# Kernel tuning notes

Hardware: AMD Instinct MI355X
Metric: run time of the kernel (lower is better)

## Reference

```python
import jax, jax.numpy as jnp
import numpy as np

WINDOW = 512
OVERLAP = 64
STRIDE = WINDOW - OVERLAP  # 448
HEADS = 12
HEAD_DIM = 3072 // HEADS  # 256
SCALE = 1.0 / np.sqrt(HEAD_DIM)


def setup_inputs() -> dict:
    key = jax.random.key(0)
    ks = jax.random.split(key, 9)
    B, S, H = 1, 8192, 3072
    w = 0.02  # weight init scale
    return {
        "hidden_states": jax.random.normal(ks[0], (B, S, H), jnp.float32),
        "Wq": jax.random.normal(ks[1], (H, H), jnp.float32) * w,
        "bq": jnp.zeros((H,), jnp.float32),
        "Wk": jax.random.normal(ks[2], (H, H), jnp.float32) * w,
        "bk": jnp.zeros((H,), jnp.float32),
        "Wv": jax.random.normal(ks[3], (H, H), jnp.float32) * w,
        "bv": jnp.zeros((H,), jnp.float32),
        "Wo": jax.random.normal(ks[4], (H, H), jnp.float32) * w,
        "bo": jnp.zeros((H,), jnp.float32),
    }


def reference(hidden_states, Wq, bq, Wk, bk, Wv, bv, Wo, bo):
    B, S, H = hidden_states.shape
    n_win = -(-S // STRIDE)  # ceil: windows start at 0, STRIDE, 2*STRIDE, ... < S
    starts = np.arange(n_win) * STRIDE                      # static
    idx = starts[:, None] + np.arange(WINDOW)[None, :]      # [n_win, W]
    valid = jnp.asarray(idx < S)                            # [n_win, W] bool
    idx_c = np.minimum(idx, S - 1)                          # clamp for gather

    # Gather overlapping windows: [B, n_win, W, H] (redundant QKV on overlap, as in original)
    win = hidden_states[:, idx_c]

    def proj(Wm, bm):
        y = jnp.einsum('bnwh,oh->bnwo', win, Wm) + bm
        return y.reshape(B, n_win, WINDOW, HEADS, HEAD_DIM)

    q = proj(Wq, bq)
    k = proj(Wk, bk)
    v = proj(Wv, bv)

    scores = jnp.einsum('bnqhd,bnkhd->bnhqk', q, k) * SCALE  # [B,n_win,heads,W,W]
    # Padded (out-of-range) key positions of the short last window must not attend
    scores = jnp.where(valid[None, :, None, None, :], scores, -1e9)
    attn = jax.nn.softmax(scores, axis=-1)
    ctx = jnp.einsum('bnhqk,bnkhd->bnqhd', attn, v)
    ctx = ctx.reshape(B, n_win, WINDOW, H)
    out_w = jnp.einsum('bnwh,oh->bnwo', ctx, Wo) + bo        # [B,n_win,W,H]

    # zero padded query rows, then overlap-add + average
    out_w = out_w * valid[None, :, :, None].astype(out_w.dtype)
    flat_idx = jnp.asarray(idx_c.reshape(-1))                # [n_win*W]
    output = jnp.zeros((B, S, H), out_w.dtype).at[:, flat_idx].add(
        out_w.reshape(B, -1, H))
    counts = jnp.zeros((S,), out_w.dtype).at[flat_idx].add(
        valid.reshape(-1).astype(out_w.dtype))
    return output / jnp.maximum(counts, 1.0)[None, :, None]
```

## Files before the change

kernel.cpp:

```cpp
#include <hip/hip_runtime.h>
#include <hip/hip_bf16.h>
#include <stdint.h>

#define SEQ   8192
#define HDIM  3072
#define NWIN  19
#define WINL  512
#define STR   448
#define NHEAD 12
#define DHEAD 256
#define QKVN  9216
#define ATTN_SCALE 0.0625f

typedef unsigned short u16;
typedef __bf16 bf16x8 __attribute__((ext_vector_type(8)));
typedef float  f32x4  __attribute__((ext_vector_type(4)));
typedef unsigned short us8 __attribute__((ext_vector_type(8)));

__device__ __forceinline__ u16 f2b(float x) {
  return __builtin_bit_cast(u16, __float2bfloat16(x));
}
__device__ __forceinline__ float b2f(u16 u) {
  return __builtin_bit_cast(float, (unsigned int)(u) << 16);
}
__device__ __forceinline__ void gload_lds16(const void* g, void* l) {
  __builtin_amdgcn_global_load_lds(
      (const __attribute__((address_space(1))) void*)g,
      (__attribute__((address_space(3))) void*)l, 16, 0, 0);
}

__global__ __launch_bounds__(256) void cvt_f32_bf16(const float* __restrict__ src,
                                                    u16* __restrict__ dst, int n8) {
  int i = blockIdx.x * 256 + threadIdx.x;
  if (i >= n8) return;
  const float4* s4 = (const float4*)src;
  float4 a = s4[2 * i], b = s4[2 * i + 1];
  us8 o;
  o[0] = f2b(a.x); o[1] = f2b(a.y); o[2] = f2b(a.z); o[3] = f2b(a.w);
  o[4] = f2b(b.x); o[5] = f2b(b.y); o[6] = f2b(b.z); o[7] = f2b(b.w);
  *((us8*)dst + i) = o;
}

__global__ __launch_bounds__(256) void biascat(const float* __restrict__ bq,
                                               const float* __restrict__ bk,
                                               const float* __restrict__ bv,
                                               float* __restrict__ dst) {
  int i = blockIdx.x * 256 + threadIdx.x;
  if (i >= QKVN) return;
  dst[i] = (i < HDIM) ? bq[i] : ((i < 2 * HDIM) ? bk[i - HDIM] : bv[i - 2 * HDIM]);
}

template <bool BF16OUT>
__global__ __launch_bounds__(512, 2) void gemm256(const u16* __restrict__ A,
                                                  const u16* __restrict__ B,
                                                  const float* __restrict__ bias,
                                                  float* __restrict__ outF,
                                                  u16* __restrict__ outB,
                                                  int N, int K) {
  __shared__ __align__(16) u16 As[2][2][128][64];
  __shared__ __align__(16) u16 Bs[2][2][128][64];
  const int tid = threadIdx.x;
  const int w = tid >> 6, l = tid & 63;
  const int wm = w >> 2, wn = w & 3;
  const int fr = l & 15, g = l >> 4;
  const int xcd = blockIdx.x & 7, loc = blockIdx.x >> 3;
  const int bn = loc >> 2, bm = xcd * 4 + (loc & 3);

  const int srow = tid >> 3;
  const int lc = (tid & 7) ^ ((tid >> 3) & 7);
  const u16* sA0 = A + (size_t)(bm * 256 + srow) * K + lc * 8;
  const u16* sA1 = sA0 + (size_t)64 * K;
  const u16* sB0 = B + (size_t)(bn * 256 + srow) * K + lc * 8;
  const u16* sB1 = sB0 + (size_t)64 * K;
  const size_t hiK = (size_t)128 * K;
  const int t16 = tid * 16;
  char* Aw = (char*)As;
  char* Bw = (char*)Bs;

  int rbA[4], rbB[2], ck[2];
#pragma unroll
  for (int i = 0; i < 4; ++i) rbA[i] = (i * 32 + wm * 16 + fr) * 128;
  rbB[0] = (wn * 16 + fr) * 128;
  rbB[1] = (64 + wn * 16 + fr) * 128;
  ck[0] = ((g) ^ (fr & 7)) * 16;
  ck[1] = ((4 + g) ^ (fr & 7)) * 16;

  f32x4 acc[8][4];
#pragma unroll
  for (int i = 0; i < 8; ++i)
#pragma unroll
    for (int j = 0; j < 4; ++j) acc[i][j] = (f32x4){0.f, 0.f, 0.f, 0.f};

  gload_lds16(sA0, Aw + t16); gload_lds16(sA1, Aw + 8192 + t16);
  gload_lds16(sB0, Bw + t16); gload_lds16(sB1, Bw + 8192 + t16);
  gload_lds16(sB0 + hiK, Bw + 16384 + t16); gload_lds16(sB1 + hiK, Bw + 16384 + 8192 + t16);
  gload_lds16(sA0 + hiK, Aw + 16384 + t16); gload_lds16(sA1 + hiK, Aw + 16384 + 8192 + t16);
  sA0 += 64; sA1 += 64; sB0 += 64; sB1 += 64;
  asm volatile("s_waitcnt vmcnt(4)" ::: "memory");
  __builtin_amdgcn_s_barrier();
  __builtin_amdgcn_sched_barrier(0);

  const int NT = K >> 6;
  for (int T = 0; T < NT; ++T) {
    const int cur = T & 1, pp = (T + 1) & 1;
    const bool ds = (T + 1 < NT);
    const bool last = (T == NT - 1);
    const char* ah = (const char*)As + cur * 32768;
    const char* bh = (const char*)Bs + cur * 32768;
    char* apw = Aw + pp * 32768;
    char* bpw = Bw + pp * 32768;
    bf16x8 af[4][2], bf[4][2];

#pragma unroll
    for (int mi = 0; mi < 4; ++mi)
#pragma unroll
      for (int kk = 0; kk < 2; ++kk)
        af[mi][kk] = *(const bf16x8*)(ah + rbA[mi] + ck[kk]);
#pragma unroll
    for (int ni = 0; ni < 2; ++ni)
#pragma unroll
      for (int kk = 0; kk < 2; ++kk)
        bf[ni][kk] = *(const bf16x8*)(bh + rbB[ni] + ck[kk]);
    if (ds) { gload_lds16(sA0, apw + t16); gload_lds16(sA1, apw + 8192 + t16); }
    __builtin_amdgcn_s_barrier();
    asm volatile("s_waitcnt lgkmcnt(0)" ::: "memory");
    __builtin_amdgcn_s_setprio(1);
#pragma unroll
    for (int kk = 0; kk < 2; ++kk)
#pragma unroll
      for (int mi = 0; mi < 4; ++mi)
#pragma unroll
        for (int ni = 0; ni < 2; ++ni)
          acc[mi][ni] = __builtin_amdgcn_mfma_f32_16x16x32_bf16(af[mi][kk], bf[ni][kk], acc[mi][ni], 0, 0, 0);
    __builtin_amdgcn_s_setprio(0);
    if (last) asm volatile("s_waitcnt vmcnt(2)" ::: "memory");
    else      asm volatile("s_waitcnt vmcnt(4)" ::: "memory");
    __builtin_amdgcn_s_barrier();

#pragma unroll
    for (int ni = 2; ni < 4; ++ni)
#pragma unroll
      for (int kk = 0; kk < 2; ++kk)
        bf[ni][kk] = *(const bf16x8*)(bh + 16384 + rbB[ni - 2] + ck[kk]);
    if (ds) { gload_lds16(sB0, bpw + t16); gload_lds16(sB1, bpw + 8192 + t16); }
    __builtin_amdgcn_s_barrier();
    asm volatile("s_waitcnt lgkmcnt(0)" ::: "memory");
    __builtin_amdgcn_s_setprio(1);
#pragma unroll
    for (int kk = 0; kk < 2; ++kk)
#pragma unroll
      for (int mi = 0; mi < 4; ++mi)
#pragma unroll
        for (int ni = 2; ni < 4; ++ni)
          acc[mi][ni] = __builtin_amdgcn_mfma_f32_16x16x32_bf16(af[mi][kk], bf[ni][kk], acc[mi][ni], 0, 0, 0);
    __builtin_amdgcn_s_setprio(0);
    if (last) asm volatile("s_waitcnt vmcnt(0)" ::: "memory");
    else      asm volatile("s_waitcnt vmcnt(4)" ::: "memory");
    __builtin_amdgcn_s_barrier();

#pragma unroll
    for (int mi = 0; mi < 4; ++mi)
#pragma unroll
      for (int kk = 0; kk < 2; ++kk)
        af[mi][kk] = *(const bf16x8*)(ah + 16384 + rbA[mi] + ck[kk]);
    if (ds) { gload_lds16(sB0 + hiK, bpw + 16384 + t16); gload_lds16(sB1 + hiK, bpw + 16384 + 8192 + t16); }
    __builtin_amdgcn_s_barrier();
    asm volatile("s_waitcnt lgkmcnt(0)" ::: "memory");
    __builtin_amdgcn_s_setprio(1);
#pragma unroll
    for (int kk = 0; kk < 2; ++kk)
#pragma unroll
      for (int mi = 0; mi < 4; ++mi)
#pragma unroll
        for (int ni = 0; ni < 2; ++ni)
          acc[mi + 4][ni] = __builtin_amdgcn_mfma_f32_16x16x32_bf16(af[mi][kk], bf[ni][kk], acc[mi + 4][ni], 0, 0, 0);
    __builtin_amdgcn_s_setprio(0);
    __builtin_amdgcn_s_barrier();

    if (ds) { gload_lds16(sA0 + hiK, apw + 16384 + t16); gload_lds16(sA1 + hiK, apw + 16384 + 8192 + t16); }
    __builtin_amdgcn_s_barrier();
    __builtin_amdgcn_s_setprio(1);
#pragma unroll
    for (int kk = 0; kk < 2; ++kk)
#pragma unroll
      for (int mi = 0; mi < 4; ++mi)
#pragma unroll
        for (int ni = 2; ni < 4; ++ni)
          acc[mi + 4][ni] = __builtin_amdgcn_mfma_f32_16x16x32_bf16(af[mi][kk], bf[ni][kk], acc[mi + 4][ni], 0, 0, 0);
    __builtin_amdgcn_s_setprio(0);
    if (!last) asm volatile("s_waitcnt vmcnt(4)" ::: "memory");
    __builtin_amdgcn_s_barrier();
    if (ds) { sA0 += 64; sA1 += 64; sB0 += 64; sB1 += 64; }
    __builtin_amdgcn_sched_barrier(0);
  }

#pragma unroll
  for (int ni = 0; ni < 4; ++ni) {
    const int c = bn * 256 + ni * 64 + wn * 16 + fr;
    const float bvv = bias ? bias[c] : 0.0f;
#pragma unroll
    for (int mi = 0; mi < 8; ++mi) {
      const int r0 = bm * 256 + mi * 32 + wm * 16 + g * 4;
#pragma unroll
      for (int jj = 0; jj < 4; ++jj) {
        float v = acc[mi][ni][jj] + bvv;
        if (BF16OUT) outB[(size_t)(r0 + jj) * N + c] = f2b(v);
        else         outF[(size_t)(r0 + jj) * N + c] = v;
      }
    }
  }
}

__global__ __launch_bounds__(256) void vtrans(const u16* __restrict__ QKV,
                                              u16* __restrict__ Vt) {
  __shared__ u16 t[64][72];
  const int tid = threadIdx.x;
  const int s0 = blockIdx.x * 64, c0 = blockIdx.y * 64;
  {
    const int r2 = tid >> 3, cc = (tid & 7) * 8;
#pragma unroll
    for (int p = 0; p < 2; ++p) {
      const int row = r2 + p * 32;
      u16 tmp[8];
      *(uint4*)tmp = *(const uint4*)(QKV + (size_t)(s0 + row) * QKVN + 2 * HDIM + c0 + cc);
#pragma unroll
      for (int j = 0; j < 8; ++j) t[row][cc + j] = tmp[j];
    }
  }
  __syncthreads();
  {
    const int cr2 = tid >> 3, sc = tid & 7;
#pragma unroll
    for (int p = 0; p < 2; ++p) {
      const int c = cr2 + p * 32;
      u16 tmp[8];
#pragma unroll
      for (int j = 0; j < 8; ++j) tmp[j] = t[sc * 8 + j][c];
      *(uint4*)(Vt + (size_t)(c0 + c) * SEQ + s0 + sc * 8) = *(uint4*)tmp;
    }
  }
}

__global__ __launch_bounds__(256, 2) void attn_kernel(const u16* __restrict__ QKV,
                                                      const u16* __restrict__ Vt,
                                                      u16* __restrict__ ctxw) {
  __shared__ __align__(16) u16 Ks[64 * 256];
  __shared__ __align__(16) u16 Vts[256 * 64];
  __shared__ __align__(16) u16 Ps[4][16 * 64];
  const int qb = blockIdx.x, h = blockIdx.y, n = blockIdx.z;
  const int tid = threadIdx.x, w = tid >> 6, l = tid & 63;
  const int g = l >> 4, fr = l & 15;
  const int s0 = n * STR;

  bf16x8 qf[8];
  {
    int sq = s0 + qb * 64 + w * 16 + fr;
    if (sq > SEQ - 1) sq = SEQ - 1;
    const u16* qbase = QKV + (size_t)sq * QKVN + h * DHEAD + g * 8;
#pragma unroll
    for (int dc = 0; dc < 8; ++dc) qf[dc] = *(const bf16x8*)(qbase + dc * 32);
  }
  f32x4 ctx[16];
#pragma unroll
  for (int dn = 0; dn < 16; ++dn) ctx[dn] = (f32x4){0.f, 0.f, 0.f, 0.f};
  float mrow[4] = {-3e38f, -3e38f, -3e38f, -3e38f};
  float lrow[4] = {0.f, 0.f, 0.f, 0.f};

  const int kr_in = l >> 5;
  const int kcp = l & 31;
  const int vr_in = l >> 3;
  const int vcp = l & 7;

  for (int kt = 0; kt < 8; ++kt) {
    const int sb = s0 + kt * 64;
#pragma unroll
    for (int i = 0; i < 8; ++i) {
      const int c = i * 4 + w;
      {
        const int krow = c * 2 + kr_in;
        const int cl = kcp ^ (krow & 31);
        int sk = sb + krow;
        if (sk > SEQ - 1) sk = SEQ - 1;
        gload_lds16(QKV + (size_t)sk * QKVN + HDIM + h * DHEAD + cl * 8, (char*)Ks + c * 1024);
      }
      {
        const int d = c * 8 + vr_in;
        const int cl = vcp ^ (d & 7);
        int sv = sb + cl * 8;
        if (sv > SEQ - 8) sv = SEQ - 8;
        gload_lds16(Vt + (size_t)(h * DHEAD + d) * SEQ + sv, (char*)Vts + c * 1024);
      }
    }
    __syncthreads();

    f32x4 sacc[4];
#pragma unroll
    for (int kn = 0; kn < 4; ++kn) sacc[kn] = (f32x4){0.f, 0.f, 0.f, 0.f};
#pragma unroll
    for (int kn = 0; kn < 4; ++kn) {
      const int krow = kn * 16 + fr;
      const char* krp = (const char*)Ks + krow * 512;
      const int rx = krow & 31;
#pragma unroll
      for (int dc = 0; dc < 8; ++dc) {
        bf16x8 kf = *(const bf16x8*)(krp + (((dc * 4 + g) ^ rx) << 4));
        sacc[kn] = __builtin_amdgcn_mfma_f32_16x16x32_bf16(qf[dc], kf, sacc[kn], 0, 0, 0);
      }
    }
    float mt[4];
#pragma unroll
    for (int kn = 0; kn < 4; ++kn) {
      const bool valid = (sb + kn * 16 + fr) < SEQ;
#pragma unroll
      for (int r = 0; r < 4; ++r) {
        float v = valid ? sacc[kn][r] * ATTN_SCALE : -1e9f;
        sacc[kn][r] = v;
        mt[r] = (kn == 0) ? v : fmaxf(mt[r], v);
      }
    }
#pragma unroll
    for (int r = 0; r < 4; ++r) {
#pragma unroll
      for (int off = 1; off < 16; off <<= 1)
        mt[r] = fmaxf(mt[r], __shfl_xor(mt[r], off, 64));
    }
    float corr[4];
#pragma unroll
    for (int r = 0; r < 4; ++r) {
      float mnew = fmaxf(mrow[r], mt[r]);
      corr[r] = __expf(mrow[r] - mnew);
      mrow[r] = mnew;
    }
    float psum[4] = {0.f, 0.f, 0.f, 0.f};
    char* pw = (char*)&Ps[w][0];
#pragma unroll
    for (int kn = 0; kn < 4; ++kn) {
#pragma unroll
      for (int r = 0; r < 4; ++r) {
        float p = __expf(sacc[kn][r] - mrow[r]);
        psum[r] += p;
        const int q = g * 4 + r;
        *(u16*)(pw + q * 128 + ((2 * (kn * 16 + fr)) ^ ((q & 7) << 4))) = f2b(p);
      }
    }
#pragma unroll
    for (int r = 0; r < 4; ++r) {
#pragma unroll
      for (int off = 1; off < 16; off <<= 1)
        psum[r] += __shfl_xor(psum[r], off, 64);
      lrow[r] = lrow[r] * corr[r] + psum[r];
    }
#pragma unroll
    for (int dn = 0; dn < 16; ++dn)
#pragma unroll
      for (int r = 0; r < 4; ++r) ctx[dn][r] *= corr[r];
    __syncthreads();

    bf16x8 pf[2];
#pragma unroll
    for (int kc = 0; kc < 2; ++kc)
      pf[kc] = *(const bf16x8*)(pw + fr * 128 + ((kc * 64 + g * 16) ^ ((fr & 7) << 4)));
#pragma unroll
    for (int dn = 0; dn < 16; ++dn) {
      const int d = dn * 16 + fr;
      const char* vrp = (const char*)Vts + d * 128;
      const int dx = d & 7;
#pragma unroll
      for (int kc = 0; kc < 2; ++kc) {
        bf16x8 vf = *(const bf16x8*)(vrp + (((kc * 4 + g) ^ dx) << 4));
        ctx[dn] = __builtin_amdgcn_mfma_f32_16x16x32_bf16(pf[kc], vf, ctx[dn], 0, 0, 0);
      }
    }
    __syncthreads();
  }
  float inv[4];
#pragma unroll
  for (int r = 0; r < 4; ++r) inv[r] = 1.0f / lrow[r];
  const int qrow0 = qb * 64 + w * 16 + g * 4;
#pragma unroll
  for (int dn = 0; dn < 16; ++dn) {
#pragma unroll
    for (int r = 0; r < 4; ++r) {
      ctxw[(size_t)(n * WINL + qrow0 + r) * HDIM + h * DHEAD + dn * 16 + fr] =
          f2b(ctx[dn][r] * inv[r]);
    }
  }
}

__global__ __launch_bounds__(256) void combine_kernel(const u16* __restrict__ ctxw,
                                                      u16* __restrict__ ctx_avg) {
  int idx = blockIdx.x * 256 + threadIdx.x;
  if (idx >= SEQ * (HDIM / 8)) return;
  const int s = idx / (HDIM / 8);
  const int cc = (idx % (HDIM / 8)) * 8;
  const int w1 = s / STR;
  const int off1 = s - w1 * STR;
  us8 a = *(const us8*)(ctxw + (size_t)(w1 * WINL + off1) * HDIM + cc);
  if (w1 >= 1 && off1 < (WINL - STR)) {
    us8 b = *(const us8*)(ctxw + (size_t)((w1 - 1) * WINL + off1 + STR) * HDIM + cc);
#pragma unroll
    for (int j = 0; j < 8; ++j) a[j] = f2b(0.5f * (b2f(a[j]) + b2f(b[j])));
  }
  *(us8*)(ctx_avg + (size_t)s * HDIM + cc) = a;
}

__global__ void ws_marker(float* out, float v) { out[0] = v; }

extern "C" void kernel_launch(void* const* d_in, const int* in_sizes, int n_in,
                              void* d_out, int out_size, void* d_ws, size_t ws_size,
                              hipStream_t stream) {
  const float* X  = (const float*)d_in[0];
  const float* Wq = (const float*)d_in[1];
  const float* bq = (const float*)d_in[2];
  const float* Wk = (const float*)d_in[3];
  const float* bk = (const float*)d_in[4];
  const float* Wv = (const float*)d_in[5];
  const float* bv = (const float*)d_in[6];
  const float* Wo = (const float*)d_in[7];
  const float* bo = (const float*)d_in[8];
  float* out = (float*)d_out;

  const size_t OFF_XB   = 0;
  const size_t OFF_WQKV = 50331648;
  const size_t OFF_WO   = 106954752;
  const size_t OFF_QKV  = 125829120;
  const size_t OFF_VT   = 276824064;
  const size_t OFF_BIAS = 327155712;
  const size_t WS_NEED  = 327192576;
  if (ws_size < WS_NEED) {
    hipMemsetAsync(d_out, 0, (size_t)out_size * 4, stream);
    ws_marker<<<1, 1, 0, stream>>>(out, (float)(ws_size / 1048576));
    return;
  }
  char* ws = (char*)d_ws;
  u16* Xb      = (u16*)(ws + OFF_XB);
  u16* Wqkvb   = (u16*)(ws + OFF_WQKV);
  u16* Wob     = (u16*)(ws + OFF_WO);
  u16* QKV     = (u16*)(ws + OFF_QKV);
  u16* Vt      = (u16*)(ws + OFF_VT);
  float* biasQ = (float*)(ws + OFF_BIAS);
  u16* ctxw    = (u16*)d_out;
  u16* ctx_avg = Xb;

  cvt_f32_bf16<<<12288, 256, 0, stream>>>(X, Xb, SEQ * HDIM / 8);
  cvt_f32_bf16<<<4608, 256, 0, stream>>>(Wq, Wqkvb, HDIM * HDIM / 8);
  cvt_f32_bf16<<<4608, 256, 0, stream>>>(Wk, Wqkvb + (size_t)HDIM * HDIM, HDIM * HDIM / 8);
  cvt_f32_bf16<<<4608, 256, 0, stream>>>(Wv, Wqkvb + (size_t)2 * HDIM * HDIM, HDIM * HDIM / 8);
  cvt_f32_bf16<<<4608, 256, 0, stream>>>(Wo, Wob, HDIM * HDIM / 8);
  biascat<<<36, 256, 0, stream>>>(bq, bk, bv, biasQ);

  gemm256<true><<<dim3((SEQ / 256) * (QKVN / 256)), 512, 0, stream>>>(
      Xb, Wqkvb, biasQ, nullptr, QKV, QKVN, HDIM);

  vtrans<<<dim3(SEQ / 64, HDIM / 64), 256, 0, stream>>>(QKV, Vt);

  attn_kernel<<<dim3(8, NHEAD, NWIN), 256, 0, stream>>>(QKV, Vt, ctxw);

  combine_kernel<<<12288, 256, 0, stream>>>(ctxw, ctx_avg);

  gemm256<false><<<dim3((SEQ / 256) * (HDIM / 256)), 512, 0, stream>>>(
      ctx_avg, Wob, bo, out, nullptr, HDIM, HDIM);
}
```

Before: 858.8 us.

## Fuse V transpose into QKV GEMM epilogue and double query rows per attention wave

The QKV GEMM epilogue now also writes the V columns transposed into the Vt buffer, which removes the separate vtrans kernel and its extra read and write of V. The attention kernel has each wave process 32 query rows instead of 16, so each K/V tile loaded into shared memory serves twice as many queries and the grid shrinks by half. Scheduling barriers are added inside the GEMM main loop. The costs are more registers in attention (double ctx accumulators), possibly lower occupancy, fewer blocks, and narrow scattered 8-byte transposed stores from the GEMM epilogue.

```diff
diff --git a/kernel.cpp b/kernel.cpp
--- a/kernel.cpp
+++ b/kernel.cpp
@@ -56,6 +56,7 @@
                                                   const float* __restrict__ bias,
                                                   float* __restrict__ outF,
                                                   u16* __restrict__ outB,
+                                                  u16* __restrict__ vtOut,
                                                   int N, int K) {
   __shared__ __align__(16) u16 As[2][2][128][64];
   __shared__ __align__(16) u16 Bs[2][2][128][64];
@@ -124,6 +125,7 @@
     if (ds) { gload_lds16(sA0, apw + t16); gload_lds16(sA1, apw + 8192 + t16); }
     __builtin_amdgcn_s_barrier();
     asm volatile("s_waitcnt lgkmcnt(0)" ::: "memory");
+    __builtin_amdgcn_sched_barrier(0);
     __builtin_amdgcn_s_setprio(1);
 #pragma unroll
     for (int kk = 0; kk < 2; ++kk)
@@ -145,6 +147,7 @@
     if (ds) { gload_lds16(sB0, bpw + t16); gload_lds16(sB1, bpw + 8192 + t16); }
     __builtin_amdgcn_s_barrier();
     asm volatile("s_waitcnt lgkmcnt(0)" ::: "memory");
+    __builtin_amdgcn_sched_barrier(0);
     __builtin_amdgcn_s_setprio(1);
 #pragma unroll
     for (int kk = 0; kk < 2; ++kk)
@@ -166,6 +169,7 @@
     if (ds) { gload_lds16(sB0 + hiK, bpw + 16384 + t16); gload_lds16(sB1 + hiK, bpw + 16384 + 8192 + t16); }
     __builtin_amdgcn_s_barrier();
     asm volatile("s_waitcnt lgkmcnt(0)" ::: "memory");
+    __builtin_amdgcn_sched_barrier(0);
     __builtin_amdgcn_s_setprio(1);
 #pragma unroll
     for (int kk = 0; kk < 2; ++kk)
@@ -198,45 +202,18 @@
   for (int ni = 0; ni < 4; ++ni) {
     const int c = bn * 256 + ni * 64 + wn * 16 + fr;
     const float bvv = bias ? bias[c] : 0.0f;
+    const bool wv = BF16OUT && (vtOut != nullptr) && (c >= 2 * HDIM);
 #pragma unroll
     for (int mi = 0; mi < 8; ++mi) {
       const int r0 = bm * 256 + mi * 32 + wm * 16 + g * 4;
+      u16 t4[4];
 #pragma unroll
       for (int jj = 0; jj < 4; ++jj) {
         float v = acc[mi][ni][jj] + bvv;
-        if (BF16OUT) outB[(size_t)(r0 + jj) * N + c] = f2b(v);
+        if (BF16OUT) { u16 b_ = f2b(v); outB[(size_t)(r0 + jj) * N + c] = b_; t4[jj] = b_; }
         else         outF[(size_t)(r0 + jj) * N + c] = v;
       }
-    }
-  }
-}
-
-__global__ __launch_bounds__(256) void vtrans(const u16* __restrict__ QKV,
-                                              u16* __restrict__ Vt) {
-  __shared__ u16 t[64][72];
-  const int tid = threadIdx.x;
-  const int s0 = blockIdx.x * 64, c0 = blockIdx.y * 64;
-  {
-    const int r2 = tid >> 3, cc = (tid & 7) * 8;
-#pragma unroll
-    for (int p = 0; p < 2; ++p) {
-      const int row = r2 + p * 32;
-      u16 tmp[8];
-      *(uint4*)tmp = *(const uint4*)(QKV + (size_t)(s0 + row) * QKVN + 2 * HDIM + c0 + cc);
-#pragma unroll
-      for (int j = 0; j < 8; ++j) t[row][cc + j] = tmp[j];
-    }
-  }
-  __syncthreads();
-  {
-    const int cr2 = tid >> 3, sc = tid & 7;
-#pragma unroll
-    for (int p = 0; p < 2; ++p) {
-      const int c = cr2 + p * 32;
-      u16 tmp[8];
-#pragma unroll
-      for (int j = 0; j < 8; ++j) tmp[j] = t[sc * 8 + j][c];
-      *(uint4*)(Vt + (size_t)(c0 + c) * SEQ + s0 + sc * 8) = *(uint4*)tmp;
+      if (wv) *(uint2*)(vtOut + (size_t)(c - 2 * HDIM) * SEQ + r0) = *(const uint2*)t4;
     }
   }
 }
@@ -246,30 +223,37 @@
                                                       u16* __restrict__ ctxw) {
   __shared__ __align__(16) u16 Ks[64 * 256];
   __shared__ __align__(16) u16 Vts[256 * 64];
-  __shared__ __align__(16) u16 Ps[4][16 * 64];
+  __shared__ __align__(16) u16 Ps[4][32 * 64];
   const int qb = blockIdx.x, h = blockIdx.y, n = blockIdx.z;
   const int tid = threadIdx.x, w = tid >> 6, l = tid & 63;
   const int g = l >> 4, fr = l & 15;
   const int s0 = n * STR;
 
-  bf16x8 qf[8];
-  {
-    int sq = s0 + qb * 64 + w * 16 + fr;
+  bf16x8 qf[2][8];
+#pragma unroll
+  for (int rg = 0; rg < 2; ++rg) {
+    int sq = s0 + qb * 128 + w * 32 + rg * 16 + fr;
     if (sq > SEQ - 1) sq = SEQ - 1;
     const u16* qbase = QKV + (size_t)sq * QKVN + h * DHEAD + g * 8;
 #pragma unroll
-    for (int dc = 0; dc < 8; ++dc) qf[dc] = *(const bf16x8*)(qbase + dc * 32);
-  }
-  f32x4 ctx[16];
-#pragma unroll
-  for (int dn = 0; dn < 16; ++dn) ctx[dn] = (f32x4){0.f, 0.f, 0.f, 0.f};
-  float mrow[4] = {-3e38f, -3e38f, -3e38f, -3e38f};
-  float lrow[4] = {0.f, 0.f, 0.f, 0.f};
+    for (int dc = 0; dc < 8; ++dc) qf[rg][dc] = *(const bf16x8*)(qbase + dc * 32);
+  }
+  f32x4 ctx[2][16];
+#pragma unroll
+  for (int rg = 0; rg < 2; ++rg)
+#pragma unroll
+    for (int dn = 0; dn < 16; ++dn) ctx[rg][dn] = (f32x4){0.f, 0.f, 0.f, 0.f};
+  float mrow[2][4], lrow[2][4];
+#pragma unroll
+  for (int rg = 0; rg < 2; ++rg)
+#pragma unroll
+    for (int r = 0; r < 4; ++r) { mrow[rg][r] = -3e38f; lrow[rg][r] = 0.f; }
 
   const int kr_in = l >> 5;
   const int kcp = l & 31;
   const int vr_in = l >> 3;
   const int vcp = l & 7;
+  char* pw = (char*)&Ps[w][0];
 
   for (int kt = 0; kt < 8; ++kt) {
     const int sb = s0 + kt * 64;
@@ -293,73 +277,79 @@
     }
     __syncthreads();
 
-    f32x4 sacc[4];
-#pragma unroll
-    for (int kn = 0; kn < 4; ++kn) sacc[kn] = (f32x4){0.f, 0.f, 0.f, 0.f};
-#pragma unroll
-    for (int kn = 0; kn < 4; ++kn) {
-      const int krow = kn * 16 + fr;
-      const char* krp = (const char*)Ks + krow * 512;
-      const int rx = krow & 31;
-#pragma unroll
-      for (int dc = 0; dc < 8; ++dc) {
-        bf16x8 kf = *(const bf16x8*)(krp + (((dc * 4 + g) ^ rx) << 4));
-        sacc[kn] = __builtin_amdgcn_mfma_f32_16x16x32_bf16(qf[dc], kf, sacc[kn], 0, 0, 0);
-      }
+#pragma unroll
+    for (int rg = 0; rg < 2; ++rg) {
+      f32x4 sacc[4];
+#pragma unroll
+      for (int kn = 0; kn < 4; ++kn) sacc[kn] = (f32x4){0.f, 0.f, 0.f, 0.f};
+#pragma unroll
+      for (int kn = 0; kn < 4; ++kn) {
+        const int krow = kn * 16 + fr;
+        const char* krp = (const char*)Ks + krow * 512;
+        const int rx = krow & 31;
+#pragma unroll
+        for (int dc = 0; dc < 8; ++dc) {
+          bf16x8 kf = *(const bf16x8*)(krp + (((dc * 4 + g) ^ rx) << 4));
+          sacc[kn] = __builtin_amdgcn_mfma_f32_16x16x32_bf16(qf[rg][dc], kf, sacc[kn], 0, 0, 0);
+        }
+      }
+      float mt[4];
+#pragma unroll
+      for (int kn = 0; kn < 4; ++kn) {
+        const bool valid = (sb + kn * 16 + fr) < SEQ;
+#pragma unroll
+        for (int r = 0; r < 4; ++r) {
+          float v = valid ? sacc[kn][r] * ATTN_SCALE : -1e9f;
+          sacc[kn][r] = v;
+          mt[r] = (kn == 0) ? v : fmaxf(mt[r], v);
+        }
+      }
+#pragma unroll
+      for (int r = 0; r < 4; ++r) {
+#pragma unroll
+        for (int off = 1; off < 16; off <<= 1)
+          mt[r] = fmaxf(mt[r], __shfl_xor(mt[r], off, 64));
+      }
+      float corr[4];
+#pragma unroll
+      for (int r = 0; r < 4; ++r) {
+        float mnew = fmaxf(mrow[rg][r], mt[r]);
+        corr[r] = __expf(mrow[rg][r] - mnew);
+        mrow[rg][r] = mnew;
+      }
+      float psum[4] = {0.f, 0.f, 0.f, 0.f};
+#pragma unroll
+      for (int kn = 0; kn < 4; ++kn) {
+#pragma unroll
+        for (int r = 0; r < 4; ++r) {
+          float p = __expf(sacc[kn][r] - mrow[rg][r]);
+          psum[r] += p;
+          const int q = rg * 16 + g * 4 + r;
+          *(u16*)(pw + q * 128 + ((2 * (kn * 16 + fr)) ^ ((q & 7) << 4))) = f2b(p);
+        }
+      }
+#pragma unroll
+      for (int r = 0; r < 4; ++r) {
+#pragma unroll
+        for (int off = 1; off < 16; off <<= 1)
+          psum[r] += __shfl_xor(psum[r], off, 64);
+        lrow[rg][r] = lrow[rg][r] * corr[r] + psum[r];
+      }
+#pragma unroll
+      for (int dn = 0; dn < 16; ++dn)
+#pragma unroll
+        for (int r = 0; r < 4; ++r) ctx[rg][dn][r] *= corr[r];
     }
-    float mt[4];
-#pragma unroll
-    for (int kn = 0; kn < 4; ++kn) {
-      const bool valid = (sb + kn * 16 + fr) < SEQ;
-#pragma unroll
-      for (int r = 0; r < 4; ++r) {
-        float v = valid ? sacc[kn][r] * ATTN_SCALE : -1e9f;
-        sacc[kn][r] = v;
-        mt[r] = (kn == 0) ? v : fmaxf(mt[r], v);
-      }
-    }
-#pragma unroll
-    for (int r = 0; r < 4; ++r) {
-#pragma unroll
-      for (int off = 1; off < 16; off <<= 1)
-        mt[r] = fmaxf(mt[r], __shfl_xor(mt[r], off, 64));
-    }
-    float corr[4];
-#pragma unroll
-    for (int r = 0; r < 4; ++r) {
-      float mnew = fmaxf(mrow[r], mt[r]);
-      corr[r] = __expf(mrow[r] - mnew);
-      mrow[r] = mnew;
-    }
-    float psum[4] = {0.f, 0.f, 0.f, 0.f};
-    char* pw = (char*)&Ps[w][0];
-#pragma unroll
-    for (int kn = 0; kn < 4; ++kn) {
-#pragma unroll
-      for (int r = 0; r < 4; ++r) {
-        float p = __expf(sacc[kn][r] - mrow[r]);
-        psum[r] += p;
-        const int q = g * 4 + r;
-        *(u16*)(pw + q * 128 + ((2 * (kn * 16 + fr)) ^ ((q & 7) << 4))) = f2b(p);
-      }
-    }
-#pragma unroll
-    for (int r = 0; r < 4; ++r) {
-#pragma unroll
-      for (int off = 1; off < 16; off <<= 1)
-        psum[r] += __shfl_xor(psum[r], off, 64);
-      lrow[r] = lrow[r] * corr[r] + psum[r];
-    }
-#pragma unroll
-    for (int dn = 0; dn < 16; ++dn)
-#pragma unroll
-      for (int r = 0; r < 4; ++r) ctx[dn][r] *= corr[r];
-    __syncthreads();
-
-    bf16x8 pf[2];
-#pragma unroll
-    for (int kc = 0; kc < 2; ++kc)
-      pf[kc] = *(const bf16x8*)(pw + fr * 128 + ((kc * 64 + g * 16) ^ ((fr & 7) << 4)));
+    asm volatile("s_waitcnt lgkmcnt(0)" ::: "memory");
+    __builtin_amdgcn_sched_barrier(0);
+
+    bf16x8 pf[2][2];
+#pragma unroll
+    for (int rg = 0; rg < 2; ++rg)
+#pragma unroll
+      for (int kc = 0; kc < 2; ++kc)
+        pf[rg][kc] = *(const bf16x8*)(pw + (rg * 16 + fr) * 128 +
+                                      ((kc * 64 + g * 16) ^ ((fr & 7) << 4)));
 #pragma unroll
     for (int dn = 0; dn < 16; ++dn) {
       const int d = dn * 16 + fr;
@@ -368,21 +358,25 @@
 #pragma unroll
       for (int kc = 0; kc < 2; ++kc) {
         bf16x8 vf = *(const bf16x8*)(vrp + (((kc * 4 + g) ^ dx) << 4));
-        ctx[dn] = __builtin_amdgcn_mfma_f32_16x16x32_bf16(pf[kc], vf, ctx[dn], 0, 0, 0);
+        ctx[0][dn] = __builtin_amdgcn_mfma_f32_16x16x32_bf16(pf[0][kc], vf, ctx[0][dn], 0, 0, 0);
+        ctx[1][dn] = __builtin_amdgcn_mfma_f32_16x16x32_bf16(pf[1][kc], vf, ctx[1][dn], 0, 0, 0);
       }
     }
     __syncthreads();
   }
-  float inv[4];
-#pragma unroll
-  for (int r = 0; r < 4; ++r) inv[r] = 1.0f / lrow[r];
-  const int qrow0 = qb * 64 + w * 16 + g * 4;
-#pragma unroll
-  for (int dn = 0; dn < 16; ++dn) {
-#pragma unroll
-    for (int r = 0; r < 4; ++r) {
-      ctxw[(size_t)(n * WINL + qrow0 + r) * HDIM + h * DHEAD + dn * 16 + fr] =
-          f2b(ctx[dn][r] * inv[r]);
+#pragma unroll
+  for (int rg = 0; rg < 2; ++rg) {
+    float inv[4];
+#pragma unroll
+    for (int r = 0; r < 4; ++r) inv[r] = 1.0f / lrow[rg][r];
+    const int qrow0 = qb * 128 + w * 32 + rg * 16 + g * 4;
+#pragma unroll
+    for (int dn = 0; dn < 16; ++dn) {
+#pragma unroll
+      for (int r = 0; r < 4; ++r) {
+        ctxw[(size_t)(n * WINL + qrow0 + r) * HDIM + h * DHEAD + dn * 16 + fr] =
+            f2b(ctx[rg][dn][r] * inv[r]);
+      }
     }
   }
 }
@@ -450,14 +444,12 @@
   biascat<<<36, 256, 0, stream>>>(bq, bk, bv, biasQ);
 
   gemm256<true><<<dim3((SEQ / 256) * (QKVN / 256)), 512, 0, stream>>>(
-      Xb, Wqkvb, biasQ, nullptr, QKV, QKVN, HDIM);
-
-  vtrans<<<dim3(SEQ / 64, HDIM / 64), 256, 0, stream>>>(QKV, Vt);
-
-  attn_kernel<<<dim3(8, NHEAD, NWIN), 256, 0, stream>>>(QKV, Vt, ctxw);
+      Xb, Wqkvb, biasQ, nullptr, QKV, Vt, QKVN, HDIM);
+
+  attn_kernel<<<dim3(4, NHEAD, NWIN), 256, 0, stream>>>(QKV, Vt, ctxw);
 
   combine_kernel<<<12288, 256, 0, stream>>>(ctxw, ctx_avg);
 
   gemm256<false><<<dim3((SEQ / 256) * (HDIM / 256)), 512, 0, stream>>>(
-      ctx_avg, Wob, bo, out, nullptr, HDIM, HDIM);
-}
+      ctx_avg, Wob, bo, out, nullptr, nullptr, HDIM, HDIM);
+}
```

Result: slower. 1.044 ms (+21.6%).

## Fuse V transpose into QKV GEMM epilogue and relax attention sync

Applied to the files above, without the earlier changes.

Removes the separate vtrans kernel by having the QKV GEMM epilogue also write the transposed V slice directly, as 4-element column chunks per thread. This drops one full read and write pass over V and a kernel launch. The GEMM gains sched_barriers after the LDS waits. In attention, the block-wide __syncthreads before reading the per-wave P tile becomes a wave-local lgkmcnt wait, since each wave reads only its own Ps buffer. The fused transpose writes are strided 8-byte stores, which may be poorly coalesced.

```diff
diff --git a/kernel.cpp b/kernel.cpp
--- a/kernel.cpp
+++ b/kernel.cpp
@@ -56,6 +56,7 @@
                                                   const float* __restrict__ bias,
                                                   float* __restrict__ outF,
                                                   u16* __restrict__ outB,
+                                                  u16* __restrict__ vtOut,
                                                   int N, int K) {
   __shared__ __align__(16) u16 As[2][2][128][64];
   __shared__ __align__(16) u16 Bs[2][2][128][64];
@@ -124,6 +125,7 @@
     if (ds) { gload_lds16(sA0, apw + t16); gload_lds16(sA1, apw + 8192 + t16); }
     __builtin_amdgcn_s_barrier();
     asm volatile("s_waitcnt lgkmcnt(0)" ::: "memory");
+    __builtin_amdgcn_sched_barrier(0);
     __builtin_amdgcn_s_setprio(1);
 #pragma unroll
     for (int kk = 0; kk < 2; ++kk)
@@ -145,6 +147,7 @@
     if (ds) { gload_lds16(sB0, bpw + t16); gload_lds16(sB1, bpw + 8192 + t16); }
     __builtin_amdgcn_s_barrier();
     asm volatile("s_waitcnt lgkmcnt(0)" ::: "memory");
+    __builtin_amdgcn_sched_barrier(0);
     __builtin_amdgcn_s_setprio(1);
 #pragma unroll
     for (int kk = 0; kk < 2; ++kk)
@@ -166,6 +169,7 @@
     if (ds) { gload_lds16(sB0 + hiK, bpw + 16384 + t16); gload_lds16(sB1 + hiK, bpw + 16384 + 8192 + t16); }
     __builtin_amdgcn_s_barrier();
     asm volatile("s_waitcnt lgkmcnt(0)" ::: "memory");
+    __builtin_amdgcn_sched_barrier(0);
     __builtin_amdgcn_s_setprio(1);
 #pragma unroll
     for (int kk = 0; kk < 2; ++kk)
@@ -198,45 +202,18 @@
   for (int ni = 0; ni < 4; ++ni) {
     const int c = bn * 256 + ni * 64 + wn * 16 + fr;
     const float bvv = bias ? bias[c] : 0.0f;
+    const bool wv = BF16OUT && (vtOut != nullptr) && (c >= 2 * HDIM);
 #pragma unroll
     for (int mi = 0; mi < 8; ++mi) {
       const int r0 = bm * 256 + mi * 32 + wm * 16 + g * 4;
+      u16 t4[4];
 #pragma unroll
       for (int jj = 0; jj < 4; ++jj) {
         float v = acc[mi][ni][jj] + bvv;
-        if (BF16OUT) outB[(size_t)(r0 + jj) * N + c] = f2b(v);
+        if (BF16OUT) { u16 b_ = f2b(v); outB[(size_t)(r0 + jj) * N + c] = b_; t4[jj] = b_; }
         else         outF[(size_t)(r0 + jj) * N + c] = v;
       }
-    }
-  }
-}
-
-__global__ __launch_bounds__(256) void vtrans(const u16* __restrict__ QKV,
-                                              u16* __restrict__ Vt) {
-  __shared__ u16 t[64][72];
-  const int tid = threadIdx.x;
-  const int s0 = blockIdx.x * 64, c0 = blockIdx.y * 64;
-  {
-    const int r2 = tid >> 3, cc = (tid & 7) * 8;
-#pragma unroll
-    for (int p = 0; p < 2; ++p) {
-      const int row = r2 + p * 32;
-      u16 tmp[8];
-      *(uint4*)tmp = *(const uint4*)(QKV + (size_t)(s0 + row) * QKVN + 2 * HDIM + c0 + cc);
-#pragma unroll
-      for (int j = 0; j < 8; ++j) t[row][cc + j] = tmp[j];
-    }
-  }
-  __syncthreads();
-  {
-    const int cr2 = tid >> 3, sc = tid & 7;
-#pragma unroll
-    for (int p = 0; p < 2; ++p) {
-      const int c = cr2 + p * 32;
-      u16 tmp[8];
-#pragma unroll
-      for (int j = 0; j < 8; ++j) tmp[j] = t[sc * 8 + j][c];
-      *(uint4*)(Vt + (size_t)(c0 + c) * SEQ + s0 + sc * 8) = *(uint4*)tmp;
+      if (wv) *(uint2*)(vtOut + (size_t)(c - 2 * HDIM) * SEQ + r0) = *(const uint2*)t4;
     }
   }
 }
@@ -270,6 +247,7 @@
   const int kcp = l & 31;
   const int vr_in = l >> 3;
   const int vcp = l & 7;
+  char* pw = (char*)&Ps[w][0];
 
   for (int kt = 0; kt < 8; ++kt) {
     const int sb = s0 + kt * 64;
@@ -332,7 +310,6 @@
       mrow[r] = mnew;
     }
     float psum[4] = {0.f, 0.f, 0.f, 0.f};
-    char* pw = (char*)&Ps[w][0];
 #pragma unroll
     for (int kn = 0; kn < 4; ++kn) {
 #pragma unroll
@@ -354,7 +331,8 @@
     for (int dn = 0; dn < 16; ++dn)
 #pragma unroll
       for (int r = 0; r < 4; ++r) ctx[dn][r] *= corr[r];
-    __syncthreads();
+    asm volatile("s_waitcnt lgkmcnt(0)" ::: "memory");
+    __builtin_amdgcn_sched_barrier(0);
 
     bf16x8 pf[2];
 #pragma unroll
@@ -450,14 +428,12 @@
   biascat<<<36, 256, 0, stream>>>(bq, bk, bv, biasQ);
 
   gemm256<true><<<dim3((SEQ / 256) * (QKVN / 256)), 512, 0, stream>>>(
-      Xb, Wqkvb, biasQ, nullptr, QKV, QKVN, HDIM);
-
-  vtrans<<<dim3(SEQ / 64, HDIM / 64), 256, 0, stream>>>(QKV, Vt);
+      Xb, Wqkvb, biasQ, nullptr, QKV, Vt, QKVN, HDIM);
 
   attn_kernel<<<dim3(8, NHEAD, NWIN), 256, 0, stream>>>(QKV, Vt, ctxw);
 
   combine_kernel<<<12288, 256, 0, stream>>>(ctxw, ctx_avg);
 
   gemm256<false><<<dim3((SEQ / 256) * (HDIM / 256)), 512, 0, stream>>>(
-      ctx_avg, Wob, bo, out, nullptr, HDIM, HDIM);
-}
+      ctx_avg, Wob, bo, out, nullptr, nullptr, HDIM, HDIM);
+}
```

New measurement: 851.4 us. About the same (-0.9%).
